# Kernel tuning notes

Hardware: AMD Instinct MI355X
Metric: run time of the kernel (lower is better)

The kernel has to match this reference:

```python
import jax, jax.numpy as jnp
import numpy as np

BN_EPS = 1e-5


def setup_inputs() -> dict:
    key = jax.random.key(0)
    ks = jax.random.split(key, 9)
    B, C, H, W = 2, 64, 128, 128
    Ci = 32  # inter_channels
    sc = 0.05
    x = jax.random.normal(ks[0], (B, C, H, W), jnp.float32)
    g_w = jax.random.normal(ks[1], (Ci, C), jnp.float32) * sc
    g_b = jax.random.normal(ks[2], (Ci,), jnp.float32) * sc
    theta_w = jax.random.normal(ks[3], (Ci, C), jnp.float32) * sc
    theta_b = jax.random.normal(ks[4], (Ci,), jnp.float32) * sc
    phi_w = jax.random.normal(ks[5], (Ci, C), jnp.float32) * sc
    phi_b = jax.random.normal(ks[6], (Ci,), jnp.float32) * sc
    w_w = jax.random.normal(ks[7], (C, Ci), jnp.float32) * sc
    w_b = jnp.zeros((C,), jnp.float32)
    # BatchNorm affine params (random so the block is non-trivial; the torch
    # code zero-inits them, which would make the whole block an identity).
    bn_gamma = 1.0 + 0.1 * jax.random.normal(ks[8], (C,), jnp.float32)
    bn_beta = jnp.zeros((C,), jnp.float32)
    return dict(x=x, g_w=g_w, g_b=g_b, theta_w=theta_w, theta_b=theta_b,
                phi_w=phi_w, phi_b=phi_b, w_w=w_w, w_b=w_b,
                bn_gamma=bn_gamma, bn_beta=bn_beta)


def reference(x, g_w, g_b, theta_w, theta_b, phi_w, phi_b, w_w, w_b,
              bn_gamma, bn_beta):
    B, C, H, W = x.shape
    Ci = g_w.shape[0]
    H1, W1 = H // 2, W // 2

    def block(xq):  # embedded-gaussian non-local block on one quadrant group [B,C,h,w]
        b, c, h, w = xq.shape
        n = h * w
        xf = xq.reshape(b, c, n)                                  # [B,C,N]
        th = jnp.einsum('oc,bcn->bno', theta_w, xf) + theta_b     # [B,N,Ci]
        ph = jnp.einsum('oc,bcn->bon', phi_w, xf) + phi_b[:, None]  # [B,Ci,N]
        gx = jnp.einsum('oc,bcn->bno', g_w, xf) + g_b             # [B,N,Ci]
        f = jnp.einsum('bno,bom->bnm', th, ph)                    # [B,N,N] affinity
        a = jax.nn.softmax(f, axis=-1)
        y = jnp.einsum('bnm,bmo->bno', a, gx)                     # [B,N,Ci]
        wy = jnp.einsum('co,bno->bcn', w_w, y) + w_b[:, None]     # [B,C,N]
        wy = wy.reshape(b, c, h, w)
        # BatchNorm2d, training-mode batch stats (per quadrant call in torch)
        mu = wy.mean(axis=(0, 2, 3), keepdims=True)
        var = wy.var(axis=(0, 2, 3), keepdims=True)
        bn = (wy - mu) * jax.lax.rsqrt(var + BN_EPS)
        bn = bn * bn_gamma[None, :, None, None] + bn_beta[None, :, None, None]
        return bn + xq                                            # residual

    # split into 4 quadrants: [B,C,H,W] -> [4,B,C,H1,W1] (quadrant-major)
    xq = x.reshape(B, C, 2, H1, 2, W1).transpose(2, 4, 0, 1, 3, 5)
    xq = xq.reshape(4, B, C, H1, W1)
    zq = jax.vmap(block)(xq)                                      # [4,B,C,H1,W1]
    # reassemble
    z = zq.reshape(2, 2, B, C, H1, W1).transpose(2, 3, 0, 4, 1, 5)
    return z.reshape(B, C, H, W)
```

## Files before the change

### kernel.cpp

```cpp
#include <hip/hip_runtime.h>
#include <stdint.h>

typedef __bf16 bf16x8 __attribute__((ext_vector_type(8)));
typedef short  short4v __attribute__((ext_vector_type(4)));
typedef float  floatx4 __attribute__((ext_vector_type(4)));
typedef uint32_t u32x4 __attribute__((ext_vector_type(4)));

#define DI __device__ __forceinline__

DI uint16_t f2bf(float f) {
    union { float f; uint32_t i; } v; v.f = f;
    uint32_t u = v.i;
    return (uint16_t)((u + 0x7FFFu + ((u >> 16) & 1u)) >> 16);
}
DI uint32_t packbf2(float a, float b) {
    return __builtin_amdgcn_perm(__float_as_uint(b) + 0x8000u,
                                 __float_as_uint(a) + 0x8000u, 0x07060302u);
}

__global__ __launch_bounds__(256) void proj_kernel(
    const float* __restrict__ x,
    const float* __restrict__ tw, const float* __restrict__ tb,
    const float* __restrict__ pw, const float* __restrict__ pb,
    const float* __restrict__ gw, const float* __restrict__ gb,
    uint16_t* __restrict__ th, uint16_t* __restrict__ phT,
    uint16_t* __restrict__ vP)
{
    __shared__ uint16_t ldsg[32 * 68];
    int nt = blockIdx.x & 63, blk = blockIdx.x >> 6;
    int tid = threadIdx.x, wid = tid >> 6, lane = tid & 63;
    int quad = lane >> 4, low = lane & 15;

    int b = blk & 1, q = blk >> 1, qh = q >> 1, qw = q & 1;
    int pixA = wid * 16 + low;
    const float* xg = x + (size_t)b * 1048576 +
                      (size_t)(qh * 64 + nt) * 128 + qw * 64 + pixA;

    float a0[8], a1[8];
#pragma unroll
    for (int j = 0; j < 8; ++j) {
        a0[j] = xg[(size_t)(quad * 8 + j) * 16384];
        a1[j] = xg[(size_t)(32 + quad * 8 + j) * 16384];
    }
    union { uint32_t u[4]; bf16x8 v; } A0, A1;
#pragma unroll
    for (int j = 0; j < 4; ++j) {
        A0.u[j] = packbf2(a0[2*j], a0[2*j+1]);
        A1.u[j] = packbf2(a1[2*j], a1[2*j+1]);
    }

    auto dotile = [&](const float* W, const float* Bv, int o0) -> floatx4 {
        floatx4 acc;
        float bias = Bv[o0 + low];
#pragma unroll
        for (int r = 0; r < 4; ++r) acc[r] = bias;
        const float* wr = W + (o0 + low) * 64 + quad * 8;
        floatx4 w0a = *(const floatx4*)(wr);
        floatx4 w0b = *(const floatx4*)(wr + 4);
        floatx4 w1a = *(const floatx4*)(wr + 32);
        floatx4 w1b = *(const floatx4*)(wr + 36);
        union { uint32_t u[4]; bf16x8 v; } B0, B1;
        B0.u[0] = packbf2(w0a[0], w0a[1]); B0.u[1] = packbf2(w0a[2], w0a[3]);
        B0.u[2] = packbf2(w0b[0], w0b[1]); B0.u[3] = packbf2(w0b[2], w0b[3]);
        B1.u[0] = packbf2(w1a[0], w1a[1]); B1.u[1] = packbf2(w1a[2], w1a[3]);
        B1.u[2] = packbf2(w1b[0], w1b[1]); B1.u[3] = packbf2(w1b[2], w1b[3]);
        acc = __builtin_amdgcn_mfma_f32_16x16x32_bf16(A0.v, B0.v, acc, 0, 0, 0);
        acc = __builtin_amdgcn_mfma_f32_16x16x32_bf16(A1.v, B1.v, acc, 0, 0, 0);
        return acc;
    };

    size_t thbase = ((size_t)blk * 4096 + nt * 64 + wid * 16 + quad * 4) * 32;

    floatx4 t0 = dotile(tw, tb, 0), t1 = dotile(tw, tb, 16);
#pragma unroll
    for (int r = 0; r < 4; ++r) {
        th[thbase + r * 32 + low]      = f2bf(t0[r] * 1.44269504088896f);
        th[thbase + r * 32 + 16 + low] = f2bf(t1[r] * 1.44269504088896f);
    }
    floatx4 p0 = dotile(pw, pb, 0), p1 = dotile(pw, pb, 16);
#pragma unroll
    for (int r = 0; r < 4; ++r) {
        phT[thbase + r * 32 + low]      = f2bf(p0[r]);
        phT[thbase + r * 32 + 16 + low] = f2bf(p1[r]);
    }
    floatx4 g0 = dotile(gw, gb, 0), g1 = dotile(gw, gb, 16);
#pragma unroll
    for (int r = 0; r < 4; ++r) {
        ldsg[(low)      * 68 + wid * 16 + quad * 4 + r] = f2bf(g0[r]);
        ldsg[(16 + low) * 68 + wid * 16 + quad * 4 + r] = f2bf(g1[r]);
    }
    __syncthreads();
    {
        int o = tid >> 3, k = (tid & 7) * 8;
        const uint16_t* src = &ldsg[o * 68 + k];
        uint64_t lo = *(const uint64_t*)(src);
        uint64_t hi = *(const uint64_t*)(src + 4);
        union { uint64_t q[2]; u32x4 v; } out;
        out.q[0] = lo; out.q[1] = hi;
        *(u32x4*)(vP + (size_t)blk * 131072 + nt * 2048 + tid * 8) = out.v;
    }
}

__global__ __launch_bounds__(256, 2) void flash_kernel(
    const uint16_t* __restrict__ th, const uint16_t* __restrict__ phT,
    const uint16_t* __restrict__ vP, const float* __restrict__ w_w,
    const float* __restrict__ w_b, float* __restrict__ wy,
    float2* __restrict__ partials)
{
    __shared__ uint16_t ldsK[2][2][64 * 40];
    __shared__ uint16_t ldsV[2][2][32 * 72];
    __shared__ float sred[4][64][2];
    int rg  = blockIdx.x & 63;
    int blk = blockIdx.x >> 6;
    int tid = threadIdx.x, wid = tid >> 6, lane = tid & 63;
    int quad = lane >> 4, low = lane & 15;
    int n0 = rg * 64 + wid * 16;

    const uint16_t* thB = th  + (size_t)blk * 131072;
    const uint16_t* kG  = phT + (size_t)blk * 131072;
    const uint16_t* vG  = vP  + (size_t)blk * 131072;

    bf16x8 qf = *(const bf16x8*)(thB + (n0 + low) * 32 + quad * 8);

    const int kWr = (tid >> 2) * 40 + (tid & 3) * 8;
    const int vWr = (tid >> 3) * 72 + (tid & 7) * 8;
    const u32x4* kSrc = (const u32x4*)kG + tid;
    const u32x4* vSrc = (const u32x4*)vG + tid;

    u32x4 kr0 = kSrc[0],  kr1 = kSrc[256];
    u32x4 vr0 = vSrc[0],  vr1 = vSrc[256];
    *(u32x4*)(&ldsK[0][0][kWr]) = kr0;  *(u32x4*)(&ldsK[0][1][kWr]) = kr1;
    *(u32x4*)(&ldsV[0][0][vWr]) = vr0;  *(u32x4*)(&ldsV[0][1][vWr]) = vr1;
    __syncthreads();

    floatx4 zero = {0.f, 0.f, 0.f, 0.f};
    floatx4 oa0 = zero, oa1 = zero, os = zero;
    union { uint32_t u[2]; short4v v; } ones;
    ones.u[0] = 0x3F803F80u; ones.u[1] = 0x3F803F80u;

    for (int t = 0; t < 32; ++t) {
        int buf = t & 1;
        if (t < 31) {
            kr0 = kSrc[(2*t + 2) * 256]; kr1 = kSrc[(2*t + 3) * 256];
            vr0 = vSrc[(2*t + 2) * 256]; vr1 = vSrc[(2*t + 3) * 256];
        }
#pragma unroll
        for (int s = 0; s < 2; ++s) {
            const uint16_t* Kb = ldsK[buf][s];
            const uint16_t* Vb = ldsV[buf][s];
            bf16x8  kf[4]; short4v va[4], vb[4];
#pragma unroll
            for (int c = 0; c < 4; ++c) {
                kf[c] = *(const bf16x8*)(Kb + (c * 16 + low) * 40 + quad * 8);
                va[c] = *(const short4v*)(Vb + low * 72 + c * 16 + quad * 4);
                vb[c] = *(const short4v*)(Vb + (16 + low) * 72 + c * 16 + quad * 4);
            }
            floatx4 sa[4];
#pragma unroll
            for (int c = 0; c < 4; ++c)
                sa[c] = __builtin_amdgcn_mfma_f32_16x16x32_bf16(kf[c], qf, zero, 0, 0, 0);
            union { uint32_t u[2]; short4v v; } P[4];
#pragma unroll
            for (int c = 0; c < 4; ++c) {
                float p0 = __builtin_amdgcn_exp2f(sa[c][0]);
                float p1 = __builtin_amdgcn_exp2f(sa[c][1]);
                float p2 = __builtin_amdgcn_exp2f(sa[c][2]);
                float p3 = __builtin_amdgcn_exp2f(sa[c][3]);
                P[c].u[0] = packbf2(p0, p1);
                P[c].u[1] = packbf2(p2, p3);
            }
#pragma unroll
            for (int c = 0; c < 4; ++c) {
                oa0 = __builtin_amdgcn_mfma_f32_16x16x16bf16_1k(va[c], P[c].v, oa0, 0, 0, 0);
                oa1 = __builtin_amdgcn_mfma_f32_16x16x16bf16_1k(vb[c], P[c].v, oa1, 0, 0, 0);
                os  = __builtin_amdgcn_mfma_f32_16x16x16bf16_1k(ones.v, P[c].v, os, 0, 0, 0);
            }
        }
        if (t < 31) {
            *(u32x4*)(&ldsK[buf ^ 1][0][kWr]) = kr0;
            *(u32x4*)(&ldsK[buf ^ 1][1][kWr]) = kr1;
            *(u32x4*)(&ldsV[buf ^ 1][0][vWr]) = vr0;
            *(u32x4*)(&ldsV[buf ^ 1][1][vWr]) = vr1;
        }
        __syncthreads();
    }

    float rinv = 1.0f / os[0];
    union { uint32_t u[2]; short4v v; } Y0, Y1;
    Y0.u[0] = packbf2(oa0[0] * rinv, oa0[1] * rinv);
    Y0.u[1] = packbf2(oa0[2] * rinv, oa0[3] * rinv);
    Y1.u[0] = packbf2(oa1[0] * rinv, oa1[1] * rinv);
    Y1.u[1] = packbf2(oa1[2] * rinv, oa1[3] * rinv);

    float* wyB = wy + (size_t)blk * 262144;
    int n = n0 + low;
#pragma unroll
    for (int ct = 0; ct < 4; ++ct) {
        floatx4 acc;
#pragma unroll
        for (int r = 0; r < 4; ++r) acc[r] = w_b[ct * 16 + quad * 4 + r];
        floatx4 w0 = *(const floatx4*)(w_w + (ct * 16 + low) * 32 + quad * 4);
        floatx4 w1 = *(const floatx4*)(w_w + (ct * 16 + low) * 32 + 16 + quad * 4);
        union { uint32_t u[2]; short4v v; } W0, W1;
        W0.u[0] = packbf2(w0[0], w0[1]); W0.u[1] = packbf2(w0[2], w0[3]);
        W1.u[0] = packbf2(w1[0], w1[1]); W1.u[1] = packbf2(w1[2], w1[3]);
        acc = __builtin_amdgcn_mfma_f32_16x16x16bf16_1k(W0.v, Y0.v, acc, 0, 0, 0);
        acc = __builtin_amdgcn_mfma_f32_16x16x16bf16_1k(W1.v, Y1.v, acc, 0, 0, 0);
#pragma unroll
        for (int r = 0; r < 4; ++r) {
            wyB[(size_t)(ct * 16 + quad * 4 + r) * 4096 + n] = acc[r];
            float s = acc[r], ss = acc[r] * acc[r];
            s += __shfl_xor(s, 1); ss += __shfl_xor(ss, 1);
            s += __shfl_xor(s, 2); ss += __shfl_xor(ss, 2);
            s += __shfl_xor(s, 4); ss += __shfl_xor(ss, 4);
            s += __shfl_xor(s, 8); ss += __shfl_xor(ss, 8);
            if (low == 0) {
                sred[wid][ct * 16 + quad * 4 + r][0] = s;
                sred[wid][ct * 16 + quad * 4 + r][1] = ss;
            }
        }
    }
    __syncthreads();
    if (tid < 64) {
        float s  = sred[0][tid][0] + sred[1][tid][0] + sred[2][tid][0] + sred[3][tid][0];
        float ss = sred[0][tid][1] + sred[1][tid][1] + sred[2][tid][1] + sred[3][tid][1];
        partials[(size_t)blockIdx.x * 64 + tid] = make_float2(s, ss);
    }
}

__global__ __launch_bounds__(256) void stats_kernel(
    const float2* __restrict__ partials, const float* __restrict__ gamma,
    const float* __restrict__ beta, float2* __restrict__ stats)
{
    int q = blockIdx.x;
    int c = threadIdx.x & 63, g = threadIdx.x >> 6;
    float S = 0.f, SS = 0.f;
    for (int w = g; w < 128; w += 4) {
        int wg = (q * 2 + (w >> 6)) * 64 + (w & 63);
        float2 p = partials[(size_t)wg * 64 + c];
        S += p.x; SS += p.y;
    }
    __shared__ float sh[2][4][64];
    sh[0][g][c] = S; sh[1][g][c] = SS;
    __syncthreads();
    if (threadIdx.x < 64) {
        int cc = threadIdx.x;
        float St  = sh[0][0][cc] + sh[0][1][cc] + sh[0][2][cc] + sh[0][3][cc];
        float SSt = sh[1][0][cc] + sh[1][1][cc] + sh[1][2][cc] + sh[1][3][cc];
        float mu  = St * (1.0f / 8192.0f);
        float var = SSt * (1.0f / 8192.0f) - mu * mu;
        float scale = gamma[cc] * rsqrtf(var + 1e-5f);
        float shift = beta[cc] - mu * scale;
        stats[q * 64 + cc] = make_float2(scale, shift);
    }
}

__global__ __launch_bounds__(256) void final_kernel(
    const float* __restrict__ wy, const float2* __restrict__ stats,
    const float* __restrict__ x, float* __restrict__ out)
{
    size_t base = ((size_t)blockIdx.x * 256 + threadIdx.x) * 4;
    int n   = (int)(base & 4095);
    int c   = (int)((base >> 12) & 63);
    int blk = (int)(base >> 18);
    int b = blk & 1, q = blk >> 1, qh = q >> 1, qw = q & 1;
    int i = n >> 6, j = n & 63;
    float2 sc = stats[q * 64 + c];
    floatx4 wv = *(const floatx4*)(wy + base);
    size_t xa = ((size_t)(b * 64 + c) * 128 + (qh * 64 + i)) * 128 + qw * 64 + j;
    floatx4 xv = *(const floatx4*)(x + xa);
    floatx4 ov;
#pragma unroll
    for (int k = 0; k < 4; ++k) ov[k] = wv[k] * sc.x + sc.y + xv[k];
    *(floatx4*)(out + xa) = ov;
}

extern "C" void kernel_launch(void* const* d_in, const int* in_sizes, int n_in,
                              void* d_out, int out_size, void* d_ws, size_t ws_size,
                              hipStream_t stream)
{
    const float* x       = (const float*)d_in[0];
    const float* g_w     = (const float*)d_in[1];
    const float* g_b     = (const float*)d_in[2];
    const float* theta_w = (const float*)d_in[3];
    const float* theta_b = (const float*)d_in[4];
    const float* phi_w   = (const float*)d_in[5];
    const float* phi_b   = (const float*)d_in[6];
    const float* w_w     = (const float*)d_in[7];
    const float* w_b     = (const float*)d_in[8];
    const float* gamma   = (const float*)d_in[9];
    const float* beta    = (const float*)d_in[10];

    char* ws = (char*)d_ws;
    uint16_t* th       = (uint16_t*)(ws);
    uint16_t* phT      = (uint16_t*)(ws + (2u << 20));
    uint16_t* vP       = (uint16_t*)(ws + (4u << 20));
    float*    wy       = (float*)(ws + (6u << 20));
    float2*   partials = (float2*)(ws + (14u << 20));
    float2*   stats    = (float2*)(ws + (14u << 20) + (1u << 18));

    proj_kernel  <<<512,  256, 0, stream>>>(x, theta_w, theta_b, phi_w, phi_b,
                                            g_w, g_b, th, phT, vP);
    flash_kernel <<<512,  256, 0, stream>>>(th, phT, vP, w_w, w_b, wy, partials);
    stats_kernel <<<4,    256, 0, stream>>>(partials, gamma, beta, stats);
    final_kernel <<<2048, 256, 0, stream>>>(wy, stats, x, (float*)d_out);
}
```

Before: 138.3 us.

## Split flash attention along keys with 32-row query tiles and merge kernel

The flash kernel now has each wave handle 32 query rows instead of 16, so every K/V tile loaded into LDS feeds twice as many MFMAs. The key dimension is split in two to keep 512 blocks. Partial unnormalized outputs and row sums go to a workspace. Row sums are taken with scalar adds plus shuffles instead of a ones-vector MFMA. A new merge kernel adds the two halves, normalizes, and applies the W projection and BN partial statistics. The cost is an extra launch and fp32 partial output traffic, with wy aliased over the dead projection buffers.

```diff
diff --git a/kernel.cpp b/kernel.cpp
--- a/kernel.cpp
+++ b/kernel.cpp
@@ -103,97 +103,140 @@
 
 __global__ __launch_bounds__(256, 2) void flash_kernel(
     const uint16_t* __restrict__ th, const uint16_t* __restrict__ phT,
-    const uint16_t* __restrict__ vP, const float* __restrict__ w_w,
-    const float* __restrict__ w_b, float* __restrict__ wy,
-    float2* __restrict__ partials)
+    const uint16_t* __restrict__ vP, float* __restrict__ ypart,
+    float* __restrict__ lsum)
 {
     __shared__ uint16_t ldsK[2][2][64 * 40];
     __shared__ uint16_t ldsV[2][2][32 * 72];
+    int rg  = blockIdx.x & 31;
+    int blk = (blockIdx.x >> 5) & 7;
+    int kc  = blockIdx.x >> 8;
+    int tid = threadIdx.x, wid = tid >> 6, lane = tid & 63;
+    int quad = lane >> 4, low = lane & 15;
+    int n0 = rg * 128 + wid * 32;
+
+    const uint16_t* thB = th  + (size_t)blk * 131072;
+    const uint16_t* kG  = phT + (size_t)blk * 131072 + (size_t)kc * 65536;
+    const uint16_t* vG  = vP  + (size_t)blk * 131072 + (size_t)kc * 65536;
+
+    bf16x8 qf0 = *(const bf16x8*)(thB + (n0 + low) * 32 + quad * 8);
+    bf16x8 qf1 = *(const bf16x8*)(thB + (n0 + 16 + low) * 32 + quad * 8);
+
+    const int kWr = (tid >> 2) * 40 + (tid & 3) * 8;
+    const int vWr = (tid >> 3) * 72 + (tid & 7) * 8;
+    const u32x4* kSrc = (const u32x4*)kG + tid;
+    const u32x4* vSrc = (const u32x4*)vG + tid;
+
+    u32x4 kr0 = kSrc[0],  kr1 = kSrc[256];
+    u32x4 vr0 = vSrc[0],  vr1 = vSrc[256];
+    *(u32x4*)(&ldsK[0][0][kWr]) = kr0;  *(u32x4*)(&ldsK[0][1][kWr]) = kr1;
+    *(u32x4*)(&ldsV[0][0][vWr]) = vr0;  *(u32x4*)(&ldsV[0][1][vWr]) = vr1;
+    __syncthreads();
+
+    floatx4 zero = {0.f, 0.f, 0.f, 0.f};
+    floatx4 oa00 = zero, oa01 = zero, oa10 = zero, oa11 = zero;
+    float psum0 = 0.f, psum1 = 0.f;
+
+    for (int t = 0; t < 16; ++t) {
+        int buf = t & 1;
+        if (t < 15) {
+            kr0 = kSrc[(2*t + 2) * 256]; kr1 = kSrc[(2*t + 3) * 256];
+            vr0 = vSrc[(2*t + 2) * 256]; vr1 = vSrc[(2*t + 3) * 256];
+        }
+#pragma unroll
+        for (int s = 0; s < 2; ++s) {
+            const uint16_t* Kb = ldsK[buf][s];
+            const uint16_t* Vb = ldsV[buf][s];
+            bf16x8  kf[4]; short4v va[4], vb[4];
+#pragma unroll
+            for (int c = 0; c < 4; ++c) {
+                kf[c] = *(const bf16x8*)(Kb + (c * 16 + low) * 40 + quad * 8);
+                va[c] = *(const short4v*)(Vb + low * 72 + c * 16 + quad * 4);
+                vb[c] = *(const short4v*)(Vb + (16 + low) * 72 + c * 16 + quad * 4);
+            }
+            floatx4 sa0[4], sa1[4];
+#pragma unroll
+            for (int c = 0; c < 4; ++c) {
+                sa0[c] = __builtin_amdgcn_mfma_f32_16x16x32_bf16(kf[c], qf0, zero, 0, 0, 0);
+                sa1[c] = __builtin_amdgcn_mfma_f32_16x16x32_bf16(kf[c], qf1, zero, 0, 0, 0);
+            }
+            union { uint32_t u[2]; short4v v; } P0[4], P1[4];
+#pragma unroll
+            for (int c = 0; c < 4; ++c) {
+                float p0 = __builtin_amdgcn_exp2f(sa0[c][0]);
+                float p1 = __builtin_amdgcn_exp2f(sa0[c][1]);
+                float p2 = __builtin_amdgcn_exp2f(sa0[c][2]);
+                float p3 = __builtin_amdgcn_exp2f(sa0[c][3]);
+                psum0 += (p0 + p1) + (p2 + p3);
+                P0[c].u[0] = packbf2(p0, p1);
+                P0[c].u[1] = packbf2(p2, p3);
+                float r0 = __builtin_amdgcn_exp2f(sa1[c][0]);
+                float r1 = __builtin_amdgcn_exp2f(sa1[c][1]);
+                float r2 = __builtin_amdgcn_exp2f(sa1[c][2]);
+                float r3 = __builtin_amdgcn_exp2f(sa1[c][3]);
+                psum1 += (r0 + r1) + (r2 + r3);
+                P1[c].u[0] = packbf2(r0, r1);
+                P1[c].u[1] = packbf2(r2, r3);
+            }
+#pragma unroll
+            for (int c = 0; c < 4; ++c) {
+                oa00 = __builtin_amdgcn_mfma_f32_16x16x16bf16_1k(va[c], P0[c].v, oa00, 0, 0, 0);
+                oa01 = __builtin_amdgcn_mfma_f32_16x16x16bf16_1k(vb[c], P0[c].v, oa01, 0, 0, 0);
+                oa10 = __builtin_amdgcn_mfma_f32_16x16x16bf16_1k(va[c], P1[c].v, oa10, 0, 0, 0);
+                oa11 = __builtin_amdgcn_mfma_f32_16x16x16bf16_1k(vb[c], P1[c].v, oa11, 0, 0, 0);
+            }
+        }
+        if (t < 15) {
+            *(u32x4*)(&ldsK[buf ^ 1][0][kWr]) = kr0;
+            *(u32x4*)(&ldsK[buf ^ 1][1][kWr]) = kr1;
+            *(u32x4*)(&ldsV[buf ^ 1][0][vWr]) = vr0;
+            *(u32x4*)(&ldsV[buf ^ 1][1][vWr]) = vr1;
+        }
+        __syncthreads();
+    }
+
+    psum0 += __shfl_xor(psum0, 16); psum0 += __shfl_xor(psum0, 32);
+    psum1 += __shfl_xor(psum1, 16); psum1 += __shfl_xor(psum1, 32);
+
+    float* yB = ypart + (size_t)(kc * 8 + blk) * 131072;
+    *(floatx4*)(yB + (size_t)(n0 + low) * 32 + quad * 4)           = oa00;
+    *(floatx4*)(yB + (size_t)(n0 + low) * 32 + 16 + quad * 4)      = oa01;
+    *(floatx4*)(yB + (size_t)(n0 + 16 + low) * 32 + quad * 4)      = oa10;
+    *(floatx4*)(yB + (size_t)(n0 + 16 + low) * 32 + 16 + quad * 4) = oa11;
+    if (quad == 0) {
+        lsum[(size_t)(kc * 8 + blk) * 4096 + n0 + low]      = psum0;
+        lsum[(size_t)(kc * 8 + blk) * 4096 + n0 + 16 + low] = psum1;
+    }
+}
+
+__global__ __launch_bounds__(256) void merge_kernel(
+    const float* __restrict__ ypart, const float* __restrict__ lsum,
+    const float* __restrict__ w_w, const float* __restrict__ w_b,
+    float* __restrict__ wy, float2* __restrict__ partials)
+{
     __shared__ float sred[4][64][2];
     int rg  = blockIdx.x & 63;
     int blk = blockIdx.x >> 6;
     int tid = threadIdx.x, wid = tid >> 6, lane = tid & 63;
     int quad = lane >> 4, low = lane & 15;
     int n0 = rg * 64 + wid * 16;
-
-    const uint16_t* thB = th  + (size_t)blk * 131072;
-    const uint16_t* kG  = phT + (size_t)blk * 131072;
-    const uint16_t* vG  = vP  + (size_t)blk * 131072;
-
-    bf16x8 qf = *(const bf16x8*)(thB + (n0 + low) * 32 + quad * 8);
-
-    const int kWr = (tid >> 2) * 40 + (tid & 3) * 8;
-    const int vWr = (tid >> 3) * 72 + (tid & 7) * 8;
-    const u32x4* kSrc = (const u32x4*)kG + tid;
-    const u32x4* vSrc = (const u32x4*)vG + tid;
-
-    u32x4 kr0 = kSrc[0],  kr1 = kSrc[256];
-    u32x4 vr0 = vSrc[0],  vr1 = vSrc[256];
-    *(u32x4*)(&ldsK[0][0][kWr]) = kr0;  *(u32x4*)(&ldsK[0][1][kWr]) = kr1;
-    *(u32x4*)(&ldsV[0][0][vWr]) = vr0;  *(u32x4*)(&ldsV[0][1][vWr]) = vr1;
-    __syncthreads();
-
-    floatx4 zero = {0.f, 0.f, 0.f, 0.f};
-    floatx4 oa0 = zero, oa1 = zero, os = zero;
-    union { uint32_t u[2]; short4v v; } ones;
-    ones.u[0] = 0x3F803F80u; ones.u[1] = 0x3F803F80u;
-
-    for (int t = 0; t < 32; ++t) {
-        int buf = t & 1;
-        if (t < 31) {
-            kr0 = kSrc[(2*t + 2) * 256]; kr1 = kSrc[(2*t + 3) * 256];
-            vr0 = vSrc[(2*t + 2) * 256]; vr1 = vSrc[(2*t + 3) * 256];
-        }
-#pragma unroll
-        for (int s = 0; s < 2; ++s) {
-            const uint16_t* Kb = ldsK[buf][s];
-            const uint16_t* Vb = ldsV[buf][s];
-            bf16x8  kf[4]; short4v va[4], vb[4];
-#pragma unroll
-            for (int c = 0; c < 4; ++c) {
-                kf[c] = *(const bf16x8*)(Kb + (c * 16 + low) * 40 + quad * 8);
-                va[c] = *(const short4v*)(Vb + low * 72 + c * 16 + quad * 4);
-                vb[c] = *(const short4v*)(Vb + (16 + low) * 72 + c * 16 + quad * 4);
-            }
-            floatx4 sa[4];
-#pragma unroll
-            for (int c = 0; c < 4; ++c)
-                sa[c] = __builtin_amdgcn_mfma_f32_16x16x32_bf16(kf[c], qf, zero, 0, 0, 0);
-            union { uint32_t u[2]; short4v v; } P[4];
-#pragma unroll
-            for (int c = 0; c < 4; ++c) {
-                float p0 = __builtin_amdgcn_exp2f(sa[c][0]);
-                float p1 = __builtin_amdgcn_exp2f(sa[c][1]);
-                float p2 = __builtin_amdgcn_exp2f(sa[c][2]);
-                float p3 = __builtin_amdgcn_exp2f(sa[c][3]);
-                P[c].u[0] = packbf2(p0, p1);
-                P[c].u[1] = packbf2(p2, p3);
-            }
-#pragma unroll
-            for (int c = 0; c < 4; ++c) {
-                oa0 = __builtin_amdgcn_mfma_f32_16x16x16bf16_1k(va[c], P[c].v, oa0, 0, 0, 0);
-                oa1 = __builtin_amdgcn_mfma_f32_16x16x16bf16_1k(vb[c], P[c].v, oa1, 0, 0, 0);
-                os  = __builtin_amdgcn_mfma_f32_16x16x16bf16_1k(ones.v, P[c].v, os, 0, 0, 0);
-            }
-        }
-        if (t < 31) {
-            *(u32x4*)(&ldsK[buf ^ 1][0][kWr]) = kr0;
-            *(u32x4*)(&ldsK[buf ^ 1][1][kWr]) = kr1;
-            *(u32x4*)(&ldsV[buf ^ 1][0][vWr]) = vr0;
-            *(u32x4*)(&ldsV[buf ^ 1][1][vWr]) = vr1;
-        }
-        __syncthreads();
-    }
-
-    float rinv = 1.0f / os[0];
+    int n = n0 + low;
+
+    const float* y0 = ypart + (size_t)blk * 131072;
+    const float* y1 = ypart + (size_t)(8 + blk) * 131072;
+    float rinv = 1.0f / (lsum[(size_t)blk * 4096 + n] +
+                         lsum[(size_t)(8 + blk) * 4096 + n]);
+    floatx4 ya0 = *(const floatx4*)(y0 + (size_t)n * 32 + quad * 4);
+    floatx4 ya1 = *(const floatx4*)(y1 + (size_t)n * 32 + quad * 4);
+    floatx4 yb0 = *(const floatx4*)(y0 + (size_t)n * 32 + 16 + quad * 4);
+    floatx4 yb1 = *(const floatx4*)(y1 + (size_t)n * 32 + 16 + quad * 4);
     union { uint32_t u[2]; short4v v; } Y0, Y1;
-    Y0.u[0] = packbf2(oa0[0] * rinv, oa0[1] * rinv);
-    Y0.u[1] = packbf2(oa0[2] * rinv, oa0[3] * rinv);
-    Y1.u[0] = packbf2(oa1[0] * rinv, oa1[1] * rinv);
-    Y1.u[1] = packbf2(oa1[2] * rinv, oa1[3] * rinv);
+    Y0.u[0] = packbf2((ya0[0]+ya1[0])*rinv, (ya0[1]+ya1[1])*rinv);
+    Y0.u[1] = packbf2((ya0[2]+ya1[2])*rinv, (ya0[3]+ya1[3])*rinv);
+    Y1.u[0] = packbf2((yb0[0]+yb1[0])*rinv, (yb0[1]+yb1[1])*rinv);
+    Y1.u[1] = packbf2((yb0[2]+yb1[2])*rinv, (yb0[3]+yb1[3])*rinv);
 
     float* wyB = wy + (size_t)blk * 262144;
-    int n = n0 + low;
 #pragma unroll
     for (int ct = 0; ct < 4; ++ct) {
         floatx4 acc;
@@ -295,13 +338,16 @@
     uint16_t* th       = (uint16_t*)(ws);
     uint16_t* phT      = (uint16_t*)(ws + (2u << 20));
     uint16_t* vP       = (uint16_t*)(ws + (4u << 20));
-    float*    wy       = (float*)(ws + (6u << 20));
-    float2*   partials = (float2*)(ws + (14u << 20));
-    float2*   stats    = (float2*)(ws + (14u << 20) + (1u << 18));
+    float*    wy       = (float*)(ws);
+    float*    ypart    = (float*)(ws + (8u << 20));
+    float*    lsum     = (float*)(ws + (16u << 20));
+    float2*   partials = (float2*)(ws + (16u << 20) + (1u << 18));
+    float2*   stats    = (float2*)(ws + (16u << 20) + (2u << 18));
 
     proj_kernel  <<<512,  256, 0, stream>>>(x, theta_w, theta_b, phi_w, phi_b,
                                             g_w, g_b, th, phT, vP);
-    flash_kernel <<<512,  256, 0, stream>>>(th, phT, vP, w_w, w_b, wy, partials);
+    flash_kernel <<<512,  256, 0, stream>>>(th, phT, vP, ypart, lsum);
+    merge_kernel <<<512,  256, 0, stream>>>(ypart, lsum, w_w, w_b, wy, partials);
     stats_kernel <<<4,    256, 0, stream>>>(partials, gamma, beta, stats);
     final_kernel <<<2048, 256, 0, stream>>>(wy, stats, x, (float*)d_out);
 }
```

After: 140.6 us. Within noise of the previous version (+1.7%).

## Fuse attention, BN stats and residual epilogue into one cooperative kernel

Applied to the files above, without the earlier changes.

Merges the flash, stats and final kernels into a single cooperative launch that uses a grid-wide sync after writing BN partial sums. Each block then reduces the stats for its quadrant and applies scale/shift plus the residual straight from registers, so the fp32 wy intermediate is never written to or read back from global memory. The softmax denominator also moves from an extra MFMA against a ones vector to a scalar sum of the exp values plus cross-lane shuffles. The costs are a grid barrier that needs all 512 blocks resident at once, redundant per-block stats reduction, and uncoalesced scalar stores in the epilogue.

```diff
diff --git a/kernel.cpp b/kernel.cpp
--- a/kernel.cpp
+++ b/kernel.cpp
@@ -1,5 +1,8 @@
 #include <hip/hip_runtime.h>
+#include <hip/hip_cooperative_groups.h>
 #include <stdint.h>
+
+namespace cg = cooperative_groups;
 
 typedef __bf16 bf16x8 __attribute__((ext_vector_type(8)));
 typedef short  short4v __attribute__((ext_vector_type(4)));
@@ -95,21 +98,24 @@
         const uint16_t* src = &ldsg[o * 68 + k];
         uint64_t lo = *(const uint64_t*)(src);
         uint64_t hi = *(const uint64_t*)(src + 4);
-        union { uint64_t q[2]; u32x4 v; } out;
-        out.q[0] = lo; out.q[1] = hi;
-        *(u32x4*)(vP + (size_t)blk * 131072 + nt * 2048 + tid * 8) = out.v;
-    }
-}
-
-__global__ __launch_bounds__(256, 2) void flash_kernel(
+        union { uint64_t q[2]; u32x4 v; } outv;
+        outv.q[0] = lo; outv.q[1] = hi;
+        *(u32x4*)(vP + (size_t)blk * 131072 + nt * 2048 + tid * 8) = outv.v;
+    }
+}
+
+__global__ __launch_bounds__(256, 2) void mega_kernel(
     const uint16_t* __restrict__ th, const uint16_t* __restrict__ phT,
     const uint16_t* __restrict__ vP, const float* __restrict__ w_w,
-    const float* __restrict__ w_b, float* __restrict__ wy,
-    float2* __restrict__ partials)
+    const float* __restrict__ w_b, const float* __restrict__ gamma,
+    const float* __restrict__ beta, const float* __restrict__ x,
+    float* __restrict__ out, float2* __restrict__ partials)
 {
     __shared__ uint16_t ldsK[2][2][64 * 40];
     __shared__ uint16_t ldsV[2][2][32 * 72];
     __shared__ float sred[4][64][2];
+    __shared__ float sh2[2][4][64];
+    __shared__ float2 stl[64];
     int rg  = blockIdx.x & 63;
     int blk = blockIdx.x >> 6;
     int tid = threadIdx.x, wid = tid >> 6, lane = tid & 63;
@@ -134,9 +140,8 @@
     __syncthreads();
 
     floatx4 zero = {0.f, 0.f, 0.f, 0.f};
-    floatx4 oa0 = zero, oa1 = zero, os = zero;
-    union { uint32_t u[2]; short4v v; } ones;
-    ones.u[0] = 0x3F803F80u; ones.u[1] = 0x3F803F80u;
+    floatx4 oa0 = zero, oa1 = zero;
+    float psum = 0.f;
 
     for (int t = 0; t < 32; ++t) {
         int buf = t & 1;
@@ -166,6 +171,7 @@
                 float p1 = __builtin_amdgcn_exp2f(sa[c][1]);
                 float p2 = __builtin_amdgcn_exp2f(sa[c][2]);
                 float p3 = __builtin_amdgcn_exp2f(sa[c][3]);
+                psum += (p0 + p1) + (p2 + p3);
                 P[c].u[0] = packbf2(p0, p1);
                 P[c].u[1] = packbf2(p2, p3);
             }
@@ -173,7 +179,6 @@
             for (int c = 0; c < 4; ++c) {
                 oa0 = __builtin_amdgcn_mfma_f32_16x16x16bf16_1k(va[c], P[c].v, oa0, 0, 0, 0);
                 oa1 = __builtin_amdgcn_mfma_f32_16x16x16bf16_1k(vb[c], P[c].v, oa1, 0, 0, 0);
-                os  = __builtin_amdgcn_mfma_f32_16x16x16bf16_1k(ones.v, P[c].v, os, 0, 0, 0);
             }
         }
         if (t < 31) {
@@ -185,31 +190,33 @@
         __syncthreads();
     }
 
-    float rinv = 1.0f / os[0];
+    psum += __shfl_xor(psum, 16);
+    psum += __shfl_xor(psum, 32);
+    float rinv = 1.0f / psum;
+
     union { uint32_t u[2]; short4v v; } Y0, Y1;
     Y0.u[0] = packbf2(oa0[0] * rinv, oa0[1] * rinv);
     Y0.u[1] = packbf2(oa0[2] * rinv, oa0[3] * rinv);
     Y1.u[0] = packbf2(oa1[0] * rinv, oa1[1] * rinv);
     Y1.u[1] = packbf2(oa1[2] * rinv, oa1[3] * rinv);
 
-    float* wyB = wy + (size_t)blk * 262144;
-    int n = n0 + low;
+    floatx4 acc[4];
 #pragma unroll
     for (int ct = 0; ct < 4; ++ct) {
-        floatx4 acc;
-#pragma unroll
-        for (int r = 0; r < 4; ++r) acc[r] = w_b[ct * 16 + quad * 4 + r];
+        floatx4 a;
+#pragma unroll
+        for (int r = 0; r < 4; ++r) a[r] = w_b[ct * 16 + quad * 4 + r];
         floatx4 w0 = *(const floatx4*)(w_w + (ct * 16 + low) * 32 + quad * 4);
         floatx4 w1 = *(const floatx4*)(w_w + (ct * 16 + low) * 32 + 16 + quad * 4);
         union { uint32_t u[2]; short4v v; } W0, W1;
         W0.u[0] = packbf2(w0[0], w0[1]); W0.u[1] = packbf2(w0[2], w0[3]);
         W1.u[0] = packbf2(w1[0], w1[1]); W1.u[1] = packbf2(w1[2], w1[3]);
-        acc = __builtin_amdgcn_mfma_f32_16x16x16bf16_1k(W0.v, Y0.v, acc, 0, 0, 0);
-        acc = __builtin_amdgcn_mfma_f32_16x16x16bf16_1k(W1.v, Y1.v, acc, 0, 0, 0);
+        a = __builtin_amdgcn_mfma_f32_16x16x16bf16_1k(W0.v, Y0.v, a, 0, 0, 0);
+        a = __builtin_amdgcn_mfma_f32_16x16x16bf16_1k(W1.v, Y1.v, a, 0, 0, 0);
+        acc[ct] = a;
 #pragma unroll
         for (int r = 0; r < 4; ++r) {
-            wyB[(size_t)(ct * 16 + quad * 4 + r) * 4096 + n] = acc[r];
-            float s = acc[r], ss = acc[r] * acc[r];
+            float s = a[r], ss = a[r] * a[r];
             s += __shfl_xor(s, 1); ss += __shfl_xor(ss, 1);
             s += __shfl_xor(s, 2); ss += __shfl_xor(ss, 2);
             s += __shfl_xor(s, 4); ss += __shfl_xor(ss, 4);
@@ -226,53 +233,47 @@
         float ss = sred[0][tid][1] + sred[1][tid][1] + sred[2][tid][1] + sred[3][tid][1];
         partials[(size_t)blockIdx.x * 64 + tid] = make_float2(s, ss);
     }
-}
-
-__global__ __launch_bounds__(256) void stats_kernel(
-    const float2* __restrict__ partials, const float* __restrict__ gamma,
-    const float* __restrict__ beta, float2* __restrict__ stats)
-{
-    int q = blockIdx.x;
-    int c = threadIdx.x & 63, g = threadIdx.x >> 6;
-    float S = 0.f, SS = 0.f;
-    for (int w = g; w < 128; w += 4) {
-        int wg = (q * 2 + (w >> 6)) * 64 + (w & 63);
-        float2 p = partials[(size_t)wg * 64 + c];
-        S += p.x; SS += p.y;
-    }
-    __shared__ float sh[2][4][64];
-    sh[0][g][c] = S; sh[1][g][c] = SS;
-    __syncthreads();
-    if (threadIdx.x < 64) {
-        int cc = threadIdx.x;
-        float St  = sh[0][0][cc] + sh[0][1][cc] + sh[0][2][cc] + sh[0][3][cc];
-        float SSt = sh[1][0][cc] + sh[1][1][cc] + sh[1][2][cc] + sh[1][3][cc];
+    __threadfence();
+
+    cg::this_grid().sync();
+
+    int q = blk >> 1;
+    {
+        int c = tid & 63, g = tid >> 6;
+        float S = 0.f, SS = 0.f;
+        for (int w = g; w < 128; w += 4) {
+            int wg = (q * 2 + (w >> 6)) * 64 + (w & 63);
+            float2 p = partials[(size_t)wg * 64 + c];
+            S += p.x; SS += p.y;
+        }
+        sh2[0][g][c] = S; sh2[1][g][c] = SS;
+    }
+    __syncthreads();
+    if (tid < 64) {
+        float St  = sh2[0][0][tid] + sh2[0][1][tid] + sh2[0][2][tid] + sh2[0][3][tid];
+        float SSt = sh2[1][0][tid] + sh2[1][1][tid] + sh2[1][2][tid] + sh2[1][3][tid];
         float mu  = St * (1.0f / 8192.0f);
         float var = SSt * (1.0f / 8192.0f) - mu * mu;
-        float scale = gamma[cc] * rsqrtf(var + 1e-5f);
-        float shift = beta[cc] - mu * scale;
-        stats[q * 64 + cc] = make_float2(scale, shift);
-    }
-}
-
-__global__ __launch_bounds__(256) void final_kernel(
-    const float* __restrict__ wy, const float2* __restrict__ stats,
-    const float* __restrict__ x, float* __restrict__ out)
-{
-    size_t base = ((size_t)blockIdx.x * 256 + threadIdx.x) * 4;
-    int n   = (int)(base & 4095);
-    int c   = (int)((base >> 12) & 63);
-    int blk = (int)(base >> 18);
-    int b = blk & 1, q = blk >> 1, qh = q >> 1, qw = q & 1;
+        float scale = gamma[tid] * rsqrtf(var + 1e-5f);
+        float shift = beta[tid] - mu * scale;
+        stl[tid] = make_float2(scale, shift);
+    }
+    __syncthreads();
+
+    int b = blk & 1, qh = q >> 1, qw = q & 1;
+    int n = n0 + low;
     int i = n >> 6, j = n & 63;
-    float2 sc = stats[q * 64 + c];
-    floatx4 wv = *(const floatx4*)(wy + base);
-    size_t xa = ((size_t)(b * 64 + c) * 128 + (qh * 64 + i)) * 128 + qw * 64 + j;
-    floatx4 xv = *(const floatx4*)(x + xa);
-    floatx4 ov;
-#pragma unroll
-    for (int k = 0; k < 4; ++k) ov[k] = wv[k] * sc.x + sc.y + xv[k];
-    *(floatx4*)(out + xa) = ov;
+    size_t sp = (size_t)(qh * 64 + i) * 128 + qw * 64 + j;
+#pragma unroll
+    for (int ct = 0; ct < 4; ++ct) {
+#pragma unroll
+        for (int r = 0; r < 4; ++r) {
+            int ch = ct * 16 + quad * 4 + r;
+            float2 sc = stl[ch];
+            size_t xa = (size_t)(b * 64 + ch) * 16384 + sp;
+            out[xa] = acc[ct][r] * sc.x + sc.y + x[xa];
+        }
+    }
 }
 
 extern "C" void kernel_launch(void* const* d_in, const int* in_sizes, int n_in,
@@ -295,13 +296,15 @@
     uint16_t* th       = (uint16_t*)(ws);
     uint16_t* phT      = (uint16_t*)(ws + (2u << 20));
     uint16_t* vP       = (uint16_t*)(ws + (4u << 20));
-    float*    wy       = (float*)(ws + (6u << 20));
-    float2*   partials = (float2*)(ws + (14u << 20));
-    float2*   stats    = (float2*)(ws + (14u << 20) + (1u << 18));
-
-    proj_kernel  <<<512,  256, 0, stream>>>(x, theta_w, theta_b, phi_w, phi_b,
-                                            g_w, g_b, th, phT, vP);
-    flash_kernel <<<512,  256, 0, stream>>>(th, phT, vP, w_w, w_b, wy, partials);
-    stats_kernel <<<4,    256, 0, stream>>>(partials, gamma, beta, stats);
-    final_kernel <<<2048, 256, 0, stream>>>(wy, stats, x, (float*)d_out);
-}
+    float2*   partials = (float2*)(ws + (6u << 20));
+    float*    outp     = (float*)d_out;
+
+    proj_kernel<<<512, 256, 0, stream>>>(x, theta_w, theta_b, phi_w, phi_b,
+                                         g_w, g_b, th, phT, vP);
+
+    void* args[] = { (void*)&th, (void*)&phT, (void*)&vP, (void*)&w_w,
+                     (void*)&w_b, (void*)&gamma, (void*)&beta, (void*)&x,
+                     (void*)&outp, (void*)&partials };
+    hipLaunchCooperativeKernel((const void*)mega_kernel, dim3(512), dim3(256),
+                               args, 0, stream);
+}
```

Result: slower. 233.3 us (+68.7%).

## Process two query tiles per wave in flash kernel with 128-thread blocks

Applied to the files above, without the earlier changes.

Each wave of the flash attention kernel now handles 32 query rows instead of 16, so every K/V fragment loaded from LDS feeds two score and two output MFMA sets. Blocks shrink to two waves (128 threads), and each thread stages twice as many global-to-LDS copies per tile. This is meant to halve LDS read traffic per unit of MFMA work and cut how often the block barrier is hit. The cost is more accumulator registers per wave and fewer waves per block, which may reduce latency hiding.

```diff
diff --git a/kernel.cpp b/kernel.cpp
--- a/kernel.cpp
+++ b/kernel.cpp
@@ -95,13 +95,13 @@
         const uint16_t* src = &ldsg[o * 68 + k];
         uint64_t lo = *(const uint64_t*)(src);
         uint64_t hi = *(const uint64_t*)(src + 4);
-        union { uint64_t q[2]; u32x4 v; } out;
-        out.q[0] = lo; out.q[1] = hi;
-        *(u32x4*)(vP + (size_t)blk * 131072 + nt * 2048 + tid * 8) = out.v;
-    }
-}
-
-__global__ __launch_bounds__(256, 2) void flash_kernel(
+        union { uint64_t q[2]; u32x4 v; } outv;
+        outv.q[0] = lo; outv.q[1] = hi;
+        *(u32x4*)(vP + (size_t)blk * 131072 + nt * 2048 + tid * 8) = outv.v;
+    }
+}
+
+__global__ __launch_bounds__(128, 2) void flash_kernel(
     const uint16_t* __restrict__ th, const uint16_t* __restrict__ phT,
     const uint16_t* __restrict__ vP, const float* __restrict__ w_w,
     const float* __restrict__ w_b, float* __restrict__ wy,
@@ -109,40 +109,56 @@
 {
     __shared__ uint16_t ldsK[2][2][64 * 40];
     __shared__ uint16_t ldsV[2][2][32 * 72];
-    __shared__ float sred[4][64][2];
+    __shared__ float sred[2][64][2];
     int rg  = blockIdx.x & 63;
     int blk = blockIdx.x >> 6;
     int tid = threadIdx.x, wid = tid >> 6, lane = tid & 63;
     int quad = lane >> 4, low = lane & 15;
-    int n0 = rg * 64 + wid * 16;
+    int n0 = rg * 64 + wid * 32;
 
     const uint16_t* thB = th  + (size_t)blk * 131072;
     const uint16_t* kG  = phT + (size_t)blk * 131072;
     const uint16_t* vG  = vP  + (size_t)blk * 131072;
 
-    bf16x8 qf = *(const bf16x8*)(thB + (n0 + low) * 32 + quad * 8);
+    bf16x8 qf0 = *(const bf16x8*)(thB + (n0 + low) * 32 + quad * 8);
+    bf16x8 qf1 = *(const bf16x8*)(thB + (n0 + 16 + low) * 32 + quad * 8);
 
     const int kWr = (tid >> 2) * 40 + (tid & 3) * 8;
     const int vWr = (tid >> 3) * 72 + (tid & 7) * 8;
     const u32x4* kSrc = (const u32x4*)kG + tid;
     const u32x4* vSrc = (const u32x4*)vG + tid;
 
-    u32x4 kr0 = kSrc[0],  kr1 = kSrc[256];
-    u32x4 vr0 = vSrc[0],  vr1 = vSrc[256];
-    *(u32x4*)(&ldsK[0][0][kWr]) = kr0;  *(u32x4*)(&ldsK[0][1][kWr]) = kr1;
-    *(u32x4*)(&ldsV[0][0][vWr]) = vr0;  *(u32x4*)(&ldsV[0][1][vWr]) = vr1;
+    u32x4 kr[4], vr[4];
+#pragma unroll
+    for (int s = 0; s < 2; ++s) {
+        kr[2*s]   = kSrc[s * 256];       kr[2*s+1] = kSrc[s * 256 + 128];
+        vr[2*s]   = vSrc[s * 256];       vr[2*s+1] = vSrc[s * 256 + 128];
+    }
+#pragma unroll
+    for (int s = 0; s < 2; ++s) {
+        *(u32x4*)(&ldsK[0][s][kWr])        = kr[2*s];
+        *(u32x4*)(&ldsK[0][s][kWr + 1280]) = kr[2*s+1];
+        *(u32x4*)(&ldsV[0][s][vWr])        = vr[2*s];
+        *(u32x4*)(&ldsV[0][s][vWr + 1152]) = vr[2*s+1];
+    }
     __syncthreads();
 
     floatx4 zero = {0.f, 0.f, 0.f, 0.f};
-    floatx4 oa0 = zero, oa1 = zero, os = zero;
+    floatx4 oa00 = zero, oa01 = zero, oa10 = zero, oa11 = zero;
+    floatx4 os0 = zero, os1 = zero;
     union { uint32_t u[2]; short4v v; } ones;
     ones.u[0] = 0x3F803F80u; ones.u[1] = 0x3F803F80u;
 
     for (int t = 0; t < 32; ++t) {
         int buf = t & 1;
         if (t < 31) {
-            kr0 = kSrc[(2*t + 2) * 256]; kr1 = kSrc[(2*t + 3) * 256];
-            vr0 = vSrc[(2*t + 2) * 256]; vr1 = vSrc[(2*t + 3) * 256];
+#pragma unroll
+            for (int s = 0; s < 2; ++s) {
+                kr[2*s]   = kSrc[(2*t + 2 + s) * 256];
+                kr[2*s+1] = kSrc[(2*t + 2 + s) * 256 + 128];
+                vr[2*s]   = vSrc[(2*t + 2 + s) * 256];
+                vr[2*s+1] = vSrc[(2*t + 2 + s) * 256 + 128];
+            }
         }
 #pragma unroll
         for (int s = 0; s < 2; ++s) {
@@ -155,75 +171,103 @@
                 va[c] = *(const short4v*)(Vb + low * 72 + c * 16 + quad * 4);
                 vb[c] = *(const short4v*)(Vb + (16 + low) * 72 + c * 16 + quad * 4);
             }
-            floatx4 sa[4];
-#pragma unroll
-            for (int c = 0; c < 4; ++c)
-                sa[c] = __builtin_amdgcn_mfma_f32_16x16x32_bf16(kf[c], qf, zero, 0, 0, 0);
-            union { uint32_t u[2]; short4v v; } P[4];
+            floatx4 sa0[4], sa1[4];
 #pragma unroll
             for (int c = 0; c < 4; ++c) {
-                float p0 = __builtin_amdgcn_exp2f(sa[c][0]);
-                float p1 = __builtin_amdgcn_exp2f(sa[c][1]);
-                float p2 = __builtin_amdgcn_exp2f(sa[c][2]);
-                float p3 = __builtin_amdgcn_exp2f(sa[c][3]);
-                P[c].u[0] = packbf2(p0, p1);
-                P[c].u[1] = packbf2(p2, p3);
-            }
+                sa0[c] = __builtin_amdgcn_mfma_f32_16x16x32_bf16(kf[c], qf0, zero, 0, 0, 0);
+                sa1[c] = __builtin_amdgcn_mfma_f32_16x16x32_bf16(kf[c], qf1, zero, 0, 0, 0);
+            }
+            union { uint32_t u[2]; short4v v; } P0[4], P1[4];
 #pragma unroll
             for (int c = 0; c < 4; ++c) {
-                oa0 = __builtin_amdgcn_mfma_f32_16x16x16bf16_1k(va[c], P[c].v, oa0, 0, 0, 0);
-                oa1 = __builtin_amdgcn_mfma_f32_16x16x16bf16_1k(vb[c], P[c].v, oa1, 0, 0, 0);
-                os  = __builtin_amdgcn_mfma_f32_16x16x16bf16_1k(ones.v, P[c].v, os, 0, 0, 0);
+                float p0 = __builtin_amdgcn_exp2f(sa0[c][0]);
+                float p1 = __builtin_amdgcn_exp2f(sa0[c][1]);
+                float p2 = __builtin_amdgcn_exp2f(sa0[c][2]);
+                float p3 = __builtin_amdgcn_exp2f(sa0[c][3]);
+                P0[c].u[0] = packbf2(p0, p1);
+                P0[c].u[1] = packbf2(p2, p3);
+                float r0 = __builtin_amdgcn_exp2f(sa1[c][0]);
+                float r1 = __builtin_amdgcn_exp2f(sa1[c][1]);
+                float r2 = __builtin_amdgcn_exp2f(sa1[c][2]);
+                float r3 = __builtin_amdgcn_exp2f(sa1[c][3]);
+                P1[c].u[0] = packbf2(r0, r1);
+                P1[c].u[1] = packbf2(r2, r3);
+            }
+#pragma unroll
+            for (int c = 0; c < 4; ++c) {
+                oa00 = __builtin_amdgcn_mfma_f32_16x16x16bf16_1k(va[c], P0[c].v, oa00, 0, 0, 0);
+                oa01 = __builtin_amdgcn_mfma_f32_16x16x16bf16_1k(vb[c], P0[c].v, oa01, 0, 0, 0);
+                os0  = __builtin_amdgcn_mfma_f32_16x16x16bf16_1k(ones.v, P0[c].v, os0, 0, 0, 0);
+                oa10 = __builtin_amdgcn_mfma_f32_16x16x16bf16_1k(va[c], P1[c].v, oa10, 0, 0, 0);
+                oa11 = __builtin_amdgcn_mfma_f32_16x16x16bf16_1k(vb[c], P1[c].v, oa11, 0, 0, 0);
+                os1  = __builtin_amdgcn_mfma_f32_16x16x16bf16_1k(ones.v, P1[c].v, os1, 0, 0, 0);
             }
         }
         if (t < 31) {
-            *(u32x4*)(&ldsK[buf ^ 1][0][kWr]) = kr0;
-            *(u32x4*)(&ldsK[buf ^ 1][1][kWr]) = kr1;
-            *(u32x4*)(&ldsV[buf ^ 1][0][vWr]) = vr0;
-            *(u32x4*)(&ldsV[buf ^ 1][1][vWr]) = vr1;
+#pragma unroll
+            for (int s = 0; s < 2; ++s) {
+                *(u32x4*)(&ldsK[buf ^ 1][s][kWr])        = kr[2*s];
+                *(u32x4*)(&ldsK[buf ^ 1][s][kWr + 1280]) = kr[2*s+1];
+                *(u32x4*)(&ldsV[buf ^ 1][s][vWr])        = vr[2*s];
+                *(u32x4*)(&ldsV[buf ^ 1][s][vWr + 1152]) = vr[2*s+1];
+            }
         }
         __syncthreads();
     }
 
-    float rinv = 1.0f / os[0];
-    union { uint32_t u[2]; short4v v; } Y0, Y1;
-    Y0.u[0] = packbf2(oa0[0] * rinv, oa0[1] * rinv);
-    Y0.u[1] = packbf2(oa0[2] * rinv, oa0[3] * rinv);
-    Y1.u[0] = packbf2(oa1[0] * rinv, oa1[1] * rinv);
-    Y1.u[1] = packbf2(oa1[2] * rinv, oa1[3] * rinv);
+    float rinv0 = 1.0f / os0[0];
+    float rinv1 = 1.0f / os1[0];
+    union { uint32_t u[2]; short4v v; } Y00, Y01, Y10, Y11;
+    Y00.u[0] = packbf2(oa00[0] * rinv0, oa00[1] * rinv0);
+    Y00.u[1] = packbf2(oa00[2] * rinv0, oa00[3] * rinv0);
+    Y01.u[0] = packbf2(oa01[0] * rinv0, oa01[1] * rinv0);
+    Y01.u[1] = packbf2(oa01[2] * rinv0, oa01[3] * rinv0);
+    Y10.u[0] = packbf2(oa10[0] * rinv1, oa10[1] * rinv1);
+    Y10.u[1] = packbf2(oa10[2] * rinv1, oa10[3] * rinv1);
+    Y11.u[0] = packbf2(oa11[0] * rinv1, oa11[1] * rinv1);
+    Y11.u[1] = packbf2(oa11[2] * rinv1, oa11[3] * rinv1);
 
     float* wyB = wy + (size_t)blk * 262144;
     int n = n0 + low;
 #pragma unroll
     for (int ct = 0; ct < 4; ++ct) {
-        floatx4 acc;
-#pragma unroll
-        for (int r = 0; r < 4; ++r) acc[r] = w_b[ct * 16 + quad * 4 + r];
+        floatx4 a0, a1;
+        float bias0 = w_b[ct * 16 + quad * 4];
+        float bias1 = w_b[ct * 16 + quad * 4 + 1];
+        float bias2 = w_b[ct * 16 + quad * 4 + 2];
+        float bias3 = w_b[ct * 16 + quad * 4 + 3];
+        a0[0] = bias0; a0[1] = bias1; a0[2] = bias2; a0[3] = bias3;
+        a1 = a0;
         floatx4 w0 = *(const floatx4*)(w_w + (ct * 16 + low) * 32 + quad * 4);
         floatx4 w1 = *(const floatx4*)(w_w + (ct * 16 + low) * 32 + 16 + quad * 4);
         union { uint32_t u[2]; short4v v; } W0, W1;
         W0.u[0] = packbf2(w0[0], w0[1]); W0.u[1] = packbf2(w0[2], w0[3]);
         W1.u[0] = packbf2(w1[0], w1[1]); W1.u[1] = packbf2(w1[2], w1[3]);
-        acc = __builtin_amdgcn_mfma_f32_16x16x16bf16_1k(W0.v, Y0.v, acc, 0, 0, 0);
-        acc = __builtin_amdgcn_mfma_f32_16x16x16bf16_1k(W1.v, Y1.v, acc, 0, 0, 0);
+        a0 = __builtin_amdgcn_mfma_f32_16x16x16bf16_1k(W0.v, Y00.v, a0, 0, 0, 0);
+        a0 = __builtin_amdgcn_mfma_f32_16x16x16bf16_1k(W1.v, Y01.v, a0, 0, 0, 0);
+        a1 = __builtin_amdgcn_mfma_f32_16x16x16bf16_1k(W0.v, Y10.v, a1, 0, 0, 0);
+        a1 = __builtin_amdgcn_mfma_f32_16x16x16bf16_1k(W1.v, Y11.v, a1, 0, 0, 0);
 #pragma unroll
         for (int r = 0; r < 4; ++r) {
-            wyB[(size_t)(ct * 16 + quad * 4 + r) * 4096 + n] = acc[r];
-            float s = acc[r], ss = acc[r] * acc[r];
+            int ch = ct * 16 + quad * 4 + r;
+            wyB[(size_t)ch * 4096 + n]      = a0[r];
+            wyB[(size_t)ch * 4096 + n + 16] = a1[r];
+            float s = a0[r] + a1[r];
+            float ss = a0[r] * a0[r] + a1[r] * a1[r];
             s += __shfl_xor(s, 1); ss += __shfl_xor(ss, 1);
             s += __shfl_xor(s, 2); ss += __shfl_xor(ss, 2);
             s += __shfl_xor(s, 4); ss += __shfl_xor(ss, 4);
             s += __shfl_xor(s, 8); ss += __shfl_xor(ss, 8);
             if (low == 0) {
-                sred[wid][ct * 16 + quad * 4 + r][0] = s;
-                sred[wid][ct * 16 + quad * 4 + r][1] = ss;
+                sred[wid][ch][0] = s;
+                sred[wid][ch][1] = ss;
             }
         }
     }
     __syncthreads();
     if (tid < 64) {
-        float s  = sred[0][tid][0] + sred[1][tid][0] + sred[2][tid][0] + sred[3][tid][0];
-        float ss = sred[0][tid][1] + sred[1][tid][1] + sred[2][tid][1] + sred[3][tid][1];
+        float s  = sred[0][tid][0] + sred[1][tid][0];
+        float ss = sred[0][tid][1] + sred[1][tid][1];
         partials[(size_t)blockIdx.x * 64 + tid] = make_float2(s, ss);
     }
 }
@@ -301,7 +345,7 @@
 
     proj_kernel  <<<512,  256, 0, stream>>>(x, theta_w, theta_b, phi_w, phi_b,
                                             g_w, g_b, th, phT, vP);
-    flash_kernel <<<512,  256, 0, stream>>>(th, phT, vP, w_w, w_b, wy, partials);
+    flash_kernel <<<512,  128, 0, stream>>>(th, phT, vP, w_w, w_b, wy, partials);
     stats_kernel <<<4,    256, 0, stream>>>(partials, gamma, beta, stats);
     final_kernel <<<2048, 256, 0, stream>>>(wy, stats, x, (float*)d_out);
 }
```

Result: slower. 149.9 us (+8.4%).
